# Kernel tuning notes

Hardware: AMD Instinct MI355X
Metric: run time of the kernel (lower is better)

## Reference

```python
import jax, jax.numpy as jnp
import numpy as np

EPS = 1e-5
K = 3          # deform conv kernel size
N = K * K      # 9 sampling points per output pixel


def conv2d(x, w, b=None):
    # x [B,C,H,W], w [O,I,kh,kw], stride 1, SAME padding (== torch padding=k//2)
    y = jax.lax.conv_general_dilated(x, w, (1, 1), 'SAME',
                                     dimension_numbers=('NCHW', 'OIHW', 'NCHW'))
    if b is not None:
        y = y + b[None, :, None, None]
    return y


def bilinear_sample(img, y, x):
    # img [B,C,H,W]; y,x [B,N,H,W] float sampling coordinates; zero padding outside.
    B, C, H, W = img.shape
    y0 = jnp.floor(y); x0 = jnp.floor(x)
    wy1 = y - y0; wy0 = 1.0 - wy1
    wx1 = x - x0; wx0 = 1.0 - wx1
    img_flat = img.reshape(B, C, H * W)

    def gather(yy, xx):
        valid = (yy >= 0) & (yy <= H - 1) & (xx >= 0) & (xx <= W - 1)
        yc = jnp.clip(yy, 0, H - 1).astype(jnp.int32)
        xc = jnp.clip(xx, 0, W - 1).astype(jnp.int32)
        idx = (yc * W + xc).reshape(B, -1)                      # [B, N*H*W]
        v = jax.vmap(lambda im, ix: im[:, ix])(img_flat, idx)   # [B, C, N*H*W]
        v = v.reshape(B, C, N, H, W)
        return v * valid[:, None].astype(img.dtype)

    v00 = gather(y0,     x0)
    v01 = gather(y0,     x0 + 1)
    v10 = gather(y0 + 1, x0)
    v11 = gather(y0 + 1, x0 + 1)
    wy0 = wy0[:, None]; wy1 = wy1[:, None]
    wx0 = wx0[:, None]; wx1 = wx1[:, None]
    return wy0 * (wx0 * v00 + wx1 * v01) + wy1 * (wx0 * v10 + wx1 * v11)


def deform_conv(x, w_off, b_off, w):
    # DeformConv2d(k=3, pad=1, stride=1, bias=False): offsets predicted by a 3x3 conv,
    # per-pixel bilinear sampling at p0 + pn + offset, then 3x3 weighted sum.
    B, C, H, W = x.shape
    off = conv2d(x, w_off, b_off)               # [B, 2N, H, W]
    dy, dx = off[:, :N], off[:, N:]
    ky, kx = jnp.meshgrid(jnp.arange(K) - 1, jnp.arange(K) - 1, indexing='ij')
    ky = ky.reshape(N).astype(x.dtype)
    kx = kx.reshape(N).astype(x.dtype)
    ii = jnp.arange(H, dtype=x.dtype)[None, None, :, None]
    jj = jnp.arange(W, dtype=x.dtype)[None, None, None, :]
    ysamp = ii + ky[None, :, None, None] + dy   # [B,N,H,W]
    xsamp = jj + kx[None, :, None, None] + dx
    s = bilinear_sample(x, ysamp, xsamp)        # [B,C,N,H,W]
    Cout = w.shape[0]
    return jnp.einsum('bcnhw,ocn->bohw', s, w.reshape(Cout, C, N))


def batchnorm_relu(x, gamma, beta):
    # train-mode BatchNorm2d (batch statistics, biased variance) + ReLU
    m = x.mean(axis=(0, 2, 3), keepdims=True)
    v = x.var(axis=(0, 2, 3), keepdims=True)
    xn = (x - m) * jax.lax.rsqrt(v + EPS)
    return jax.nn.relu(xn * gamma[None, :, None, None] + beta[None, :, None, None])


def maxpool2(x):
    return jax.lax.reduce_window(x, -jnp.inf, jax.lax.max,
                                 (1, 1, 2, 2), (1, 1, 2, 2), 'VALID')


def setup_inputs() -> dict:
    key = jax.random.key(0)
    ks = jax.random.split(key, 16)
    B, Cin, Cout, H, W = 4, 32, 64, 256, 256
    Hp, Wp = H // 2, W // 2
    f = jax.random.normal
    inp = {
        'x':  f(ks[0], (B, Cin, H, W), jnp.float32),
        'h0': f(ks[1], (B, Cout, Hp, Wp), jnp.float32),
        'c0': f(ks[2], (B, Cout, Hp, Wp), jnp.float32),
        # deform conv 1: Cin -> Cout
        'w_off1': f(ks[3], (2 * N, Cin, K, K), jnp.float32) * 0.01,
        'b_off1': jnp.zeros((2 * N,), jnp.float32),
        'w1': f(ks[4], (Cout, Cin, K, K), jnp.float32) * 0.05,
        'g1': jnp.ones((Cout,), jnp.float32),
        'be1': jnp.zeros((Cout,), jnp.float32),
        # deform conv 2: Cout -> Cout
        'w_off2': f(ks[5], (2 * N, Cout, K, K), jnp.float32) * 0.01,
        'b_off2': jnp.zeros((2 * N,), jnp.float32),
        'w2': f(ks[6], (Cout, Cout, K, K), jnp.float32) * 0.05,
        'g2': jnp.ones((Cout,), jnp.float32),
        'be2': jnp.zeros((Cout,), jnp.float32),
        # ConvLSTM gates: conv(cat(x, h)) -> 4*hidden channels
        'w_gates': f(ks[7], (4 * Cout, 2 * Cout, K, K), jnp.float32) * 0.05,
        'b_gates': jnp.zeros((4 * Cout,), jnp.float32),
    }
    return inp


def reference(x, h0, c0, w_off1, b_off1, w1, g1, be1,
              w_off2, b_off2, w2, g2, be2, w_gates, b_gates):
    # maxpool_conv = MaxPool2d(2) -> DoubleDConv (deform conv + BN + ReLU, twice)
    x = maxpool2(x)
    x = batchnorm_relu(deform_conv(x, w_off1, b_off1, w1), g1, be1)
    x = batchnorm_relu(deform_conv(x, w_off2, b_off2, w2), g2, be2)
    # ConvLSTM cell
    gates = conv2d(jnp.concatenate([x, h0], axis=1), w_gates, b_gates)
    i, f, o, g = jnp.split(gates, 4, axis=1)
    c = jax.nn.sigmoid(f) * c0 + jax.nn.sigmoid(i) * jnp.tanh(g)
    h = jax.nn.sigmoid(o) * jnp.tanh(c)
    # module returns (x, state) with x == hidden, state == (hidden, cell)
    return h, c
```

## Files before the change

### kernel.cpp

```cpp
#include <hip/hip_runtime.h>
#include <hip/hip_fp16.h>
#include <math.h>

#define P 128
#define NP (P*P)
#define BATCH 4

typedef __attribute__((ext_vector_type(8))) short bf16x8;
typedef __attribute__((ext_vector_type(8))) _Float16 h16x8;
typedef __attribute__((ext_vector_type(4))) float f32x4;

__device__ __forceinline__ float sigmoidf_(float x){ return 1.f/(1.f+__expf(-x)); }
__device__ __forceinline__ float tanhf_(float x){
  float ax = fabsf(x);
  float e = __expf(2.f*ax);
  float t = 1.f - 2.f/(e + 1.f);
  return copysignf(t, x);
}
__device__ __forceinline__ short f2bf(float f){
  unsigned u = __builtin_bit_cast(unsigned, f);
  u = (u + 0x7FFFu + ((u>>16)&1u)) >> 16;
  return (short)u;
}
__device__ __forceinline__ short f2h(float f){
  return (short)__half_as_short(__float2half(f));
}

__global__ void prep_k(const float* __restrict__ x, float* __restrict__ xp,
                       const float* __restrict__ wg, const float* __restrict__ w1,
                       const float* __restrict__ w2, const float* __restrict__ wo1,
                       const float* __restrict__ wo2,
                       short* __restrict__ wA, short* __restrict__ wd1T,
                       short* __restrict__ wd2T, short* __restrict__ woT1,
                       short* __restrict__ woT2){
  int bx = blockIdx.x;
  if (bx < 256){
    int idx = bx*256 + threadIdx.x;
    int wp = idx & (P-1); int t = idx >> 7; int hp = t & (P-1); int b = t >> 7;
    const float* src = x + ((size_t)b*32*65536) + (size_t)(hp*2)*256 + wp*2;
    float m[32];
    #pragma unroll
    for (int c = 0; c < 32; c++){
      const float* s = src + (size_t)c*65536;
      float2 t0 = *(const float2*)s;
      float2 t1 = *(const float2*)(s + 256);
      m[c] = fmaxf(fmaxf(t0.x, t0.y), fmaxf(t1.x, t1.y));
    }
    float* dst = xp + (size_t)idx*32;
    #pragma unroll
    for (int q = 0; q < 8; q++) *(float4*)(dst + q*4) = *(float4*)(m + q*4);
    return;
  }
  int idx = (bx - 256)*256 + threadIdx.x;
  if (idx < 294912){
    int s = idx & 7; int l = (idx>>3) & 63; int mb = (idx>>9) & 15;
    int cb = (idx>>13) & 3; int tap = idx >> 15;
    int ln = l & 15, kg = l >> 4;
    int r = mb*16 + ln; int ch = r >> 2, gate = r & 3;
    int cin = cb*32 + kg*8 + s;
    wA[idx] = f2bf(wg[((size_t)(gate*64 + ch)*128 + cin)*9 + tap]);
    return;
  }
  idx -= 294912;
  if (idx < 18432){
    int s = idx & 7; int l = (idx>>3) & 63; int mb = (idx>>9) & 3; int tap = idx >> 11;
    int ln = l & 15, kg = l >> 4;
    int o = mb*16 + ln; int cin = kg*8 + s;
    wd1T[idx] = f2h(w1[((size_t)(o*32 + cin))*9 + tap]);
    return;
  }
  idx -= 18432;
  if (idx < 36864){
    int s = idx & 7; int l = (idx>>3) & 63; int mb = (idx>>9) & 3;
    int cb = (idx>>11) & 1; int tap = idx >> 12;
    int ln = l & 15, kg = l >> 4;
    int o = mb*16 + ln; int cin = cb*32 + kg*8 + s;
    wd2T[idx] = f2h(w2[((size_t)(o*64 + cin))*9 + tap]);
    return;
  }
  idx -= 36864;
  if (idx < 9216){
    int s = idx & 7; int l = (idx>>3) & 63; int mb = (idx>>9) & 1; int tap = idx >> 10;
    int ln = l & 15, kg = l >> 4;
    int o = mb*16 + ln; int cin = kg*8 + s;
    woT1[idx] = (o < 18) ? f2h(wo1[((size_t)(o*32 + cin))*9 + tap]) : (short)0;
    return;
  }
  idx -= 9216;
  if (idx < 18432){
    int s = idx & 7; int l = (idx>>3) & 63; int mb = (idx>>9) & 1;
    int cb = (idx>>10) & 1; int tap = idx >> 11;
    int ln = l & 15, kg = l >> 4;
    int o = mb*16 + ln; int cin = cb*32 + kg*8 + s;
    woT2[idx] = (o < 18) ? f2h(wo2[((size_t)(o*64 + cin))*9 + tap]) : (short)0;
  }
}

template<int CIN, bool BNIN>
__global__ __launch_bounds__(256) void deform_fused_k(
    const float* __restrict__ incl, const float* __restrict__ bstats,
    const float* __restrict__ b_off,
    const short* __restrict__ woT, const short* __restrict__ wdT,
    float* __restrict__ outcl, float* __restrict__ part){
  const int HS = 14, NHP = HS*HS;
  const int ROWB = CIN*2;
  const int CG = CIN/8, CGS = (CIN==64)?3:2;
  const int PM = (CIN==64)?7:3;
  const int NCB = CIN/32;
  __shared__ short xt[NHP*CIN];
  __shared__ float off_lds[64][20];
  __shared__ float red_s[4][64], red_q[4][64];
  int tid = threadIdx.x;
  int tile = blockIdx.x, b = blockIdx.y;
  int tx0 = (tile & 15)*8, ty0 = (tile >> 4)*8;
  const float* inb = incl + (size_t)b*NP*CIN;
  for (int e = tid; e < NHP*CG; e += 256){
    int cg = e & (CG-1), p = e >> CGS;
    int hr = p/HS, wc = p - hr*HS;
    int gy = ty0 + hr - 3, gx = tx0 + wc - 3;
    union { short s[8]; __half2 h[4]; h16x8 v; } u;
    if (((unsigned)gy < P) && ((unsigned)gx < P)){
      const float* src = inb + ((size_t)gy*P + gx)*CIN + cg*8;
      float4 a = *(const float4*)src, bb = *(const float4*)(src+4);
      if (BNIN){
        int c = cg*8;
        a.x = fmaxf(a.x*bstats[c+0]+bstats[64+c+0], 0.f);
        a.y = fmaxf(a.y*bstats[c+1]+bstats[64+c+1], 0.f);
        a.z = fmaxf(a.z*bstats[c+2]+bstats[64+c+2], 0.f);
        a.w = fmaxf(a.w*bstats[c+3]+bstats[64+c+3], 0.f);
        bb.x = fmaxf(bb.x*bstats[c+4]+bstats[64+c+4], 0.f);
        bb.y = fmaxf(bb.y*bstats[c+5]+bstats[64+c+5], 0.f);
        bb.z = fmaxf(bb.z*bstats[c+6]+bstats[64+c+6], 0.f);
        bb.w = fmaxf(bb.w*bstats[c+7]+bstats[64+c+7], 0.f);
      }
      u.h[0] = __float22half2_rn(float2{a.x, a.y});
      u.h[1] = __float22half2_rn(float2{a.z, a.w});
      u.h[2] = __float22half2_rn(float2{bb.x, bb.y});
      u.h[3] = __float22half2_rn(float2{bb.z, bb.w});
    } else {
      #pragma unroll
      for (int j = 0; j < 8; j++) u.s[j] = 0;
    }
    *(h16x8*)((char*)xt + p*ROWB + ((cg*16) ^ ((p & PM)<<4))) = u.v;
  }
  __syncthreads();

  int lane = tid & 63, wid = tid >> 6;
  int kg = lane >> 4, ln = lane & 15;
  int py = ty0 + wid*2 + (ln>>3), pxg = tx0 + (ln&7);
  int pl = wid*16 + ln;

  {
    f32x4 acc_o[2];
    acc_o[0] = (f32x4){0.f,0.f,0.f,0.f};
    acc_o[1] = (f32x4){0.f,0.f,0.f,0.f};
    #pragma unroll
    for (int tap = 0; tap < 9; tap++){
      int ky = tap/3, kx = tap - (tap/3)*3;
      int lr = wid*2 + (ln>>3) + ky + 2;
      int lc = (ln&7) + kx + 2;
      int p = lr*HS + lc;
      #pragma unroll
      for (int cb = 0; cb < NCB; cb++){
        h16x8 bfv = *(const h16x8*)((const char*)xt + p*ROWB + (((cb*64) + kg*16) ^ ((p & PM)<<4)));
        h16x8 af0 = *(const h16x8*)(const void*)(woT + ((size_t)((tap*NCB + cb)*2 + 0)*512 + lane*8));
        h16x8 af1 = *(const h16x8*)(const void*)(woT + ((size_t)((tap*NCB + cb)*2 + 1)*512 + lane*8));
        acc_o[0] = __builtin_amdgcn_mfma_f32_16x16x32_f16(af0, bfv, acc_o[0], 0, 0, 0);
        acc_o[1] = __builtin_amdgcn_mfma_f32_16x16x32_f16(af1, bfv, acc_o[1], 0, 0, 0);
      }
    }
    #pragma unroll
    for (int mf = 0; mf < 2; mf++){
      #pragma unroll
      for (int j = 0; j < 4; j++){
        int o = mf*16 + kg*4 + j;
        if (o < 18) off_lds[pl][o] = acc_o[mf][j] + b_off[o];
      }
    }
  }
  __syncthreads();

  f32x4 acc[4];
  #pragma unroll
  for (int mf = 0; mf < 4; mf++) acc[mf] = (f32x4){0.f,0.f,0.f,0.f};

  for (int tap = 0; tap < 9; tap++){
    float dy = off_lds[pl][tap], dx = off_lds[pl][9+tap];
    float ys = (float)(py + tap/3 - 1) + dy;
    float xs = (float)(pxg + tap%3 - 1) + dx;
    float y0f = floorf(ys), x0f = floorf(xs);
    float wy1 = ys - y0f, wx1 = xs - x0f;
    float wy0 = 1.f - wy1, wx0 = 1.f - wx1;
    int y0 = (int)y0f, x0 = (int)x0f;
    bool v0y = ((unsigned)y0 < P), v1y = ((unsigned)(y0+1) < P);
    bool v0x = ((unsigned)x0 < P), v1x = ((unsigned)(x0+1) < P);
    float w00 = (v0y && v0x) ? wy0*wx0 : 0.f;
    float w01 = (v0y && v1x) ? wy0*wx1 : 0.f;
    float w10 = (v1y && v0x) ? wy1*wx0 : 0.f;
    float w11 = (v1y && v1x) ? wy1*wx1 : 0.f;
    __half2 w00h = __float2half2_rn(w00);
    __half2 w01h = __float2half2_rn(w01);
    __half2 w10h = __float2half2_rn(w10);
    __half2 w11h = __float2half2_rn(w11);
    int ly0 = min(max(y0 - ty0 + 3, 0), HS-1);
    int ly1 = min(max(y0 + 1 - ty0 + 3, 0), HS-1);
    int lx0 = min(max(x0 - tx0 + 3, 0), HS-1);
    int lx1 = min(max(x0 + 1 - tx0 + 3, 0), HS-1);
    int p00 = ly0*HS + lx0, p01 = ly0*HS + lx1;
    int p10 = ly1*HS + lx0, p11 = ly1*HS + lx1;
    #pragma unroll
    for (int cb = 0; cb < NCB; cb++){
      int ko = (cb*32 + kg*8)*2;
      union { __half2 h[4]; h16x8 v; } c00, c01, c10, c11, bu;
      c00.v = *(const h16x8*)((const char*)xt + p00*ROWB + (ko ^ ((p00 & PM)<<4)));
      c01.v = *(const h16x8*)((const char*)xt + p01*ROWB + (ko ^ ((p01 & PM)<<4)));
      c10.v = *(const h16x8*)((const char*)xt + p10*ROWB + (ko ^ ((p10 & PM)<<4)));
      c11.v = *(const h16x8*)((const char*)xt + p11*ROWB + (ko ^ ((p11 & PM)<<4)));
      #pragma unroll
      for (int j = 0; j < 4; j++){
        bu.h[j] = __hfma2(c00.h[j], w00h,
                  __hfma2(c01.h[j], w01h,
                  __hfma2(c10.h[j], w10h,
                  __hmul2(c11.h[j], w11h))));
      }
      #pragma unroll
      for (int mf = 0; mf < 4; mf++){
        h16x8 af = *(const h16x8*)(const void*)(wdT + ((size_t)((tap*NCB + cb)*4 + mf)*512 + lane*8));
        acc[mf] = __builtin_amdgcn_mfma_f32_16x16x32_f16(af, bu.v, acc[mf], 0, 0, 0);
      }
    }
  }
  #pragma unroll
  for (int mf = 0; mf < 4; mf++){
    float* dst = outcl + ((size_t)b*NP + (size_t)py*P + pxg)*64 + mf*16 + kg*4;
    *(f32x4*)dst = acc[mf];
  }

  #pragma unroll
  for (int mf = 0; mf < 4; mf++){
    #pragma unroll
    for (int j = 0; j < 4; j++){
      float s = acc[mf][j], q = s*s;
      #pragma unroll
      for (int o = 1; o < 16; o <<= 1){
        s += __shfl_xor(s, o);
        q += __shfl_xor(q, o);
      }
      if (ln == 0){
        int ch = mf*16 + kg*4 + j;
        red_s[wid][ch] = s;
        red_q[wid][ch] = q;
      }
    }
  }
  __syncthreads();
  int blk = b*256 + tile;
  if (tid < 128){
    int ch = tid & 63;
    float v = (tid < 64)
      ? (red_s[0][ch]+red_s[1][ch]+red_s[2][ch]+red_s[3][ch])
      : (red_q[0][ch]+red_q[1][ch]+red_q[2][ch]+red_q[3][ch]);
    part[(size_t)tid*1024 + blk] = v;
  }
}

__global__ void bnfinal2_k(const float* __restrict__ part, const float* __restrict__ g,
                           const float* __restrict__ be, float* __restrict__ stats){
  int ch = blockIdx.x;
  int tid = threadIdx.x;
  float S = 0.f, Q = 0.f;
  for (int i = tid; i < 1024; i += 256){
    S += part[(size_t)ch*1024 + i];
    Q += part[(size_t)(64+ch)*1024 + i];
  }
  __shared__ float rs[256], rq[256];
  rs[tid] = S; rq[tid] = Q;
  __syncthreads();
  for (int o = 128; o > 0; o >>= 1){
    if (tid < o){ rs[tid] += rs[tid+o]; rq[tid] += rq[tid+o]; }
    __syncthreads();
  }
  if (tid == 0){
    const float inv = 1.f/(float)(BATCH*NP);
    float mean = rs[0]*inv;
    float var = rq[0]*inv - mean*mean;
    float scale = rsqrtf(var + 1e-5f)*g[ch];
    stats[ch] = scale;
    stats[64+ch] = be[ch] - mean*scale;
  }
}

__global__ void aux1_k(const float* __restrict__ part, const float* __restrict__ g,
                       const float* __restrict__ be, float* __restrict__ stats,
                       const float* __restrict__ h0, short* __restrict__ hcl){
  int bx = blockIdx.x;
  int tid = threadIdx.x;
  if (bx < 64){
    int ch = bx;
    float S = 0.f, Q = 0.f;
    for (int i = tid; i < 1024; i += 256){
      S += part[(size_t)ch*1024 + i];
      Q += part[(size_t)(64+ch)*1024 + i];
    }
    __shared__ float rs[256], rq[256];
    rs[tid] = S; rq[tid] = Q;
    __syncthreads();
    for (int o = 128; o > 0; o >>= 1){
      if (tid < o){ rs[tid] += rs[tid+o]; rq[tid] += rq[tid+o]; }
      __syncthreads();
    }
    if (tid == 0){
      const float inv = 1.f/(float)(BATCH*NP);
      float mean = rs[0]*inv;
      float var = rq[0]*inv - mean*mean;
      float scale = rsqrtf(var + 1e-5f)*g[ch];
      stats[ch] = scale;
      stats[64+ch] = be[ch] - mean*scale;
    }
    return;
  }
  {
    __shared__ float t[64][65];
    int blk = bx - 64;
    int b = blk >> 8;
    int p0 = (blk & 255)*64;
    int pl = tid & 63;
    int cq = tid >> 6;
    const float* src = h0 + (size_t)b*64*NP + p0 + pl;
    #pragma unroll
    for (int i = 0; i < 16; i++)
      t[cq*16+i][pl] = src[(size_t)(cq*16+i)*NP];
    __syncthreads();
    int p = tid >> 2, q = tid & 3;
    short* dst = hcl + ((size_t)(b*NP + p0 + p))*64 + q*16;
    union { short s[8]; bf16x8 v; } o0, o1;
    #pragma unroll
    for (int i = 0; i < 8; i++){ o0.s[i] = f2bf(t[q*16+i][p]); o1.s[i] = f2bf(t[q*16+8+i][p]); }
    *(bf16x8*)dst = o0.v;
    *(bf16x8*)(dst+8) = o1.v;
  }
}

__global__ __launch_bounds__(512, 4) void gates_mfma_k(
    const float* __restrict__ y2, const float* __restrict__ stats,
    const short* __restrict__ hcl, const float* __restrict__ c0,
    const short* __restrict__ wA, const float* __restrict__ bg,
    float* __restrict__ outh, float* __restrict__ outc){
  extern __shared__ short lds[];
  short* bs = lds;
  short* abuf = lds + 180*128;
  int tid = threadIdx.x;
  int tile = blockIdx.x, b = blockIdx.y;
  int tx0 = (tile & 7)*16, ty0 = (tile >> 3)*8;
  int lane = tid & 63, wid = tid >> 6;

  for (int e = tid; e < 180*16; e += 512){
    int cg = e & 15, p = e >> 4;
    int hr = p/18, wc = p - hr*18;
    int gy = ty0 + hr - 1, gx = tx0 + wc - 1;
    union { short s[8]; bf16x8 v; } u;
    if (((unsigned)gy < P) && ((unsigned)gx < P)){
      if (cg < 8){
        const float* src = y2 + ((size_t)(b*NP) + (size_t)gy*P + gx)*64 + cg*8;
        float4 a = *(const float4*)src, b4 = *(const float4*)(src+4);
        int c = cg*8;
        u.s[0] = f2bf(fmaxf(a.x*stats[c+0]+stats[64+c+0], 0.f));
        u.s[1] = f2bf(fmaxf(a.y*stats[c+1]+stats[64+c+1], 0.f));
        u.s[2] = f2bf(fmaxf(a.z*stats[c+2]+stats[64+c+2], 0.f));
        u.s[3] = f2bf(fmaxf(a.w*stats[c+3]+stats[64+c+3], 0.f));
        u.s[4] = f2bf(fmaxf(b4.x*stats[c+4]+stats[64+c+4], 0.f));
        u.s[5] = f2bf(fmaxf(b4.y*stats[c+5]+stats[64+c+5], 0.f));
        u.s[6] = f2bf(fmaxf(b4.z*stats[c+6]+stats[64+c+6], 0.f));
        u.s[7] = f2bf(fmaxf(b4.w*stats[c+7]+stats[64+c+7], 0.f));
      } else {
        u.v = *(const bf16x8*)(hcl + ((size_t)(b*NP) + (size_t)gy*P + gx)*64 + (cg-8)*8);
      }
    } else {
      #pragma unroll
      for (int j = 0; j < 8; j++) u.s[j] = 0;
    }
    *(bf16x8*)((char*)bs + p*256 + ((cg*16) ^ ((p&7)<<4))) = u.v;
  }

  auto stageA = [&](int c, int bi){
    const short* g = wA + (size_t)c*8192;
    short* l = abuf + bi*8192;
    #pragma unroll
    for (int i = 0; i < 2; i++){
      int unit = wid*2 + i;
      __builtin_amdgcn_global_load_lds(
          (const __attribute__((address_space(1))) unsigned int*)(g + (size_t)(unit*64 + lane)*8),
          (__attribute__((address_space(3))) unsigned int*)(l + (size_t)unit*512),
          16, 0, 0);
    }
  };

  stageA(0, 0);
  stageA(1, 1);
  __syncthreads();

  int kg = lane >> 4, ln = lane & 15;
  int ct = wid >> 1, nh = wid & 1;
  f32x4 acc[4][4];
  #pragma unroll
  for (int mf = 0; mf < 4; mf++)
    #pragma unroll
    for (int rr = 0; rr < 4; rr++) acc[mf][rr] = (f32x4){0.f,0.f,0.f,0.f};

  for (int c = 0; c < 36; c++){
    int cur = c & 1;
    int tap = c >> 2, cb = c & 3;
    int ky = tap/3, kx = tap - ky*3;
    const short* al = abuf + cur*8192;
    bf16x8 af[4], bf[4];
    #pragma unroll
    for (int mf = 0; mf < 4; mf++)
      af[mf] = *(const bf16x8*)(al + (size_t)(ct*4 + mf)*512 + lane*8);
    #pragma unroll
    for (int rr = 0; rr < 4; rr++){
      int p = (nh*4 + rr + ky)*18 + ln + kx;
      bf[rr] = *(const bf16x8*)((const char*)bs + p*256 + (((cb*64) + kg*16) ^ ((p&7)<<4)));
    }
    asm volatile("s_waitcnt lgkmcnt(0)" ::: "memory");
    __builtin_amdgcn_sched_barrier(0);
    __builtin_amdgcn_s_setprio(1);
    #pragma unroll
    for (int rr = 0; rr < 4; rr++)
      #pragma unroll
      for (int mf = 0; mf < 4; mf++)
        acc[mf][rr] = __builtin_amdgcn_mfma_f32_16x16x32_bf16(af[mf], bf[rr], acc[mf][rr], 0, 0, 0);
    __builtin_amdgcn_s_setprio(0);
    asm volatile("s_waitcnt vmcnt(0)" ::: "memory");
    __builtin_amdgcn_sched_barrier(0);
    __builtin_amdgcn_s_barrier();
    __builtin_amdgcn_sched_barrier(0);
    if (c + 2 < 36) stageA(c + 2, cur);
  }

  #pragma unroll
  for (int mf = 0; mf < 4; mf++){
    int ch = ct*16 + mf*4 + kg;
    float bi = bg[ch], bff = bg[64+ch], bo = bg[128+ch], bgv = bg[192+ch];
    #pragma unroll
    for (int rr = 0; rr < 4; rr++){
      int py = ty0 + nh*4 + rr, px = tx0 + ln;
      size_t pidx = ((size_t)(b*64 + ch))*NP + (size_t)py*P + px;
      f32x4 a = acc[mf][rr];
      float cv = sigmoidf_(a[1]+bff)*c0[pidx] + sigmoidf_(a[0]+bi)*tanhf_(a[3]+bgv);
      float hv = sigmoidf_(a[2]+bo)*tanhf_(cv);
      outh[pidx] = hv;
      outc[pidx] = cv;
    }
  }
}

extern "C" void kernel_launch(void* const* d_in, const int* in_sizes, int n_in,
                              void* d_out, int out_size, void* d_ws, size_t ws_size,
                              hipStream_t stream) {
  const float* x      = (const float*)d_in[0];
  const float* h0     = (const float*)d_in[1];
  const float* c0     = (const float*)d_in[2];
  const float* w_off1 = (const float*)d_in[3];
  const float* b_off1 = (const float*)d_in[4];
  const float* w1     = (const float*)d_in[5];
  const float* g1     = (const float*)d_in[6];
  const float* be1    = (const float*)d_in[7];
  const float* w_off2 = (const float*)d_in[8];
  const float* b_off2 = (const float*)d_in[9];
  const float* w2     = (const float*)d_in[10];
  const float* g2     = (const float*)d_in[11];
  const float* be2    = (const float*)d_in[12];
  const float* wg     = (const float*)d_in[13];
  const float* bg     = (const float*)d_in[14];

  float* ws     = (float*)d_ws;
  float* xpcl   = ws;
  short* hcl    = (short*)ws;
  float* y1     = ws + 2097152;
  float* y2     = ws + 6291456;
  float* part   = ws + 10485760;
  float* stats1 = ws + 10616832;
  float* stats2 = ws + 10616960;
  short* wA     = (short*)(ws + 10617088);
  short* wd1T   = wA + 294912;
  short* wd2T   = wd1T + 18432;
  short* woT1   = wd2T + 36864;
  short* woT2   = woT1 + 9216;

  (void)hipFuncSetAttribute((const void*)gates_mfma_k,
                            hipFuncAttributeMaxDynamicSharedMemorySize, 78848);

  prep_k<<<dim3(256 + 1476), dim3(256), 0, stream>>>(
      x, xpcl, wg, w1, w2, w_off1, w_off2, wA, wd1T, wd2T, woT1, woT2);

  deform_fused_k<32,false><<<dim3(256, BATCH), dim3(256), 0, stream>>>(
      xpcl, stats1, b_off1, woT1, wd1T, y1, part);
  aux1_k<<<dim3(64 + 1024), dim3(256), 0, stream>>>(part, g1, be1, stats1, h0, hcl);

  deform_fused_k<64,true><<<dim3(256, BATCH), dim3(256), 0, stream>>>(
      y1, stats1, b_off2, woT2, wd2T, y2, part);
  bnfinal2_k<<<dim3(64), dim3(256), 0, stream>>>(part, g2, be2, stats2);

  float* outh = (float*)d_out;
  float* outc = outh + (size_t)BATCH*64*NP;
  gates_mfma_k<<<dim3(128, BATCH), dim3(512), 78848, stream>>>(
      y2, stats2, hcl, c0, wA, bg, outh, outc);
}
```

Measured before the change: 118.0 us.

## Store deform-conv intermediates in bf16 and double-step gates MFMA pipeline

The two deform-conv outputs are now written as bf16 instead of fp32. The second deform kernel and the gates kernel read them as bf16, which halves the intermediate global traffic and workspace. The gates GEMM loop now processes two K-chunks per iteration, staging both A buffers after one barrier, to cut barrier count. This adds bf16 rounding of pre-BN activations, which may slightly change accuracy.

```diff
diff --git a/kernel.cpp b/kernel.cpp
--- a/kernel.cpp
+++ b/kernel.cpp
@@ -7,6 +7,7 @@
 #define BATCH 4
 
 typedef __attribute__((ext_vector_type(8))) short bf16x8;
+typedef __attribute__((ext_vector_type(4))) short s16x4;
 typedef __attribute__((ext_vector_type(8))) _Float16 h16x8;
 typedef __attribute__((ext_vector_type(4))) float f32x4;
 
@@ -21,6 +22,10 @@
   unsigned u = __builtin_bit_cast(unsigned, f);
   u = (u + 0x7FFFu + ((u>>16)&1u)) >> 16;
   return (short)u;
+}
+__device__ __forceinline__ float bf2f(short s){
+  unsigned u = ((unsigned)(unsigned short)s) << 16;
+  return __builtin_bit_cast(float, u);
 }
 __device__ __forceinline__ short f2h(float f){
   return (short)__half_as_short(__float2half(f));
@@ -96,12 +101,12 @@
   }
 }
 
-template<int CIN, bool BNIN>
+template<int CIN, bool BNIN, bool INBF16>
 __global__ __launch_bounds__(256) void deform_fused_k(
-    const float* __restrict__ incl, const float* __restrict__ bstats,
+    const void* __restrict__ incl, const float* __restrict__ bstats,
     const float* __restrict__ b_off,
     const short* __restrict__ woT, const short* __restrict__ wdT,
-    float* __restrict__ outcl, float* __restrict__ part){
+    short* __restrict__ outb, float* __restrict__ part){
   const int HS = 14, NHP = HS*HS;
   const int ROWB = CIN*2;
   const int CG = CIN/8, CGS = (CIN==64)?3:2;
@@ -113,30 +118,33 @@
   int tid = threadIdx.x;
   int tile = blockIdx.x, b = blockIdx.y;
   int tx0 = (tile & 15)*8, ty0 = (tile >> 4)*8;
-  const float* inb = incl + (size_t)b*NP*CIN;
   for (int e = tid; e < NHP*CG; e += 256){
     int cg = e & (CG-1), p = e >> CGS;
     int hr = p/HS, wc = p - hr*HS;
     int gy = ty0 + hr - 3, gx = tx0 + wc - 3;
     union { short s[8]; __half2 h[4]; h16x8 v; } u;
     if (((unsigned)gy < P) && ((unsigned)gx < P)){
-      const float* src = inb + ((size_t)gy*P + gx)*CIN + cg*8;
-      float4 a = *(const float4*)src, bb = *(const float4*)(src+4);
+      float v[8];
+      if (INBF16){
+        const short* src = (const short*)incl + ((size_t)b*NP + (size_t)gy*P + gx)*CIN + cg*8;
+        bf16x8 raw = *(const bf16x8*)src;
+        #pragma unroll
+        for (int j = 0; j < 8; j++) v[j] = bf2f(raw[j]);
+      } else {
+        const float* src = (const float*)incl + ((size_t)b*NP + (size_t)gy*P + gx)*CIN + cg*8;
+        float4 a = *(const float4*)src, bb = *(const float4*)(src+4);
+        v[0]=a.x; v[1]=a.y; v[2]=a.z; v[3]=a.w;
+        v[4]=bb.x; v[5]=bb.y; v[6]=bb.z; v[7]=bb.w;
+      }
       if (BNIN){
         int c = cg*8;
-        a.x = fmaxf(a.x*bstats[c+0]+bstats[64+c+0], 0.f);
-        a.y = fmaxf(a.y*bstats[c+1]+bstats[64+c+1], 0.f);
-        a.z = fmaxf(a.z*bstats[c+2]+bstats[64+c+2], 0.f);
-        a.w = fmaxf(a.w*bstats[c+3]+bstats[64+c+3], 0.f);
-        bb.x = fmaxf(bb.x*bstats[c+4]+bstats[64+c+4], 0.f);
-        bb.y = fmaxf(bb.y*bstats[c+5]+bstats[64+c+5], 0.f);
-        bb.z = fmaxf(bb.z*bstats[c+6]+bstats[64+c+6], 0.f);
-        bb.w = fmaxf(bb.w*bstats[c+7]+bstats[64+c+7], 0.f);
-      }
-      u.h[0] = __float22half2_rn(float2{a.x, a.y});
-      u.h[1] = __float22half2_rn(float2{a.z, a.w});
-      u.h[2] = __float22half2_rn(float2{bb.x, bb.y});
-      u.h[3] = __float22half2_rn(float2{bb.z, bb.w});
+        #pragma unroll
+        for (int j = 0; j < 8; j++) v[j] = fmaxf(v[j]*bstats[c+j]+bstats[64+c+j], 0.f);
+      }
+      u.h[0] = __float22half2_rn(float2{v[0], v[1]});
+      u.h[1] = __float22half2_rn(float2{v[2], v[3]});
+      u.h[2] = __float22half2_rn(float2{v[4], v[5]});
+      u.h[3] = __float22half2_rn(float2{v[6], v[7]});
     } else {
       #pragma unroll
       for (int j = 0; j < 8; j++) u.s[j] = 0;
@@ -232,8 +240,11 @@
   }
   #pragma unroll
   for (int mf = 0; mf < 4; mf++){
-    float* dst = outcl + ((size_t)b*NP + (size_t)py*P + pxg)*64 + mf*16 + kg*4;
-    *(f32x4*)dst = acc[mf];
+    short* dst = outb + ((size_t)b*NP + (size_t)py*P + pxg)*64 + mf*16 + kg*4;
+    s16x4 o;
+    #pragma unroll
+    for (int j = 0; j < 4; j++) o[j] = f2bf(acc[mf][j]);
+    *(s16x4*)dst = o;
   }
 
   #pragma unroll
@@ -342,7 +353,7 @@
 }
 
 __global__ __launch_bounds__(512, 4) void gates_mfma_k(
-    const float* __restrict__ y2, const float* __restrict__ stats,
+    const short* __restrict__ y2b, const float* __restrict__ stats,
     const short* __restrict__ hcl, const float* __restrict__ c0,
     const short* __restrict__ wA, const float* __restrict__ bg,
     float* __restrict__ outh, float* __restrict__ outc){
@@ -361,17 +372,14 @@
     union { short s[8]; bf16x8 v; } u;
     if (((unsigned)gy < P) && ((unsigned)gx < P)){
       if (cg < 8){
-        const float* src = y2 + ((size_t)(b*NP) + (size_t)gy*P + gx)*64 + cg*8;
-        float4 a = *(const float4*)src, b4 = *(const float4*)(src+4);
+        const short* src = y2b + ((size_t)(b*NP) + (size_t)gy*P + gx)*64 + cg*8;
+        bf16x8 raw = *(const bf16x8*)src;
         int c = cg*8;
-        u.s[0] = f2bf(fmaxf(a.x*stats[c+0]+stats[64+c+0], 0.f));
-        u.s[1] = f2bf(fmaxf(a.y*stats[c+1]+stats[64+c+1], 0.f));
-        u.s[2] = f2bf(fmaxf(a.z*stats[c+2]+stats[64+c+2], 0.f));
-        u.s[3] = f2bf(fmaxf(a.w*stats[c+3]+stats[64+c+3], 0.f));
-        u.s[4] = f2bf(fmaxf(b4.x*stats[c+4]+stats[64+c+4], 0.f));
-        u.s[5] = f2bf(fmaxf(b4.y*stats[c+5]+stats[64+c+5], 0.f));
-        u.s[6] = f2bf(fmaxf(b4.z*stats[c+6]+stats[64+c+6], 0.f));
-        u.s[7] = f2bf(fmaxf(b4.w*stats[c+7]+stats[64+c+7], 0.f));
+        #pragma unroll
+        for (int j = 0; j < 8; j++){
+          float v = fmaxf(bf2f(raw[j])*stats[c+j] + stats[64+c+j], 0.f);
+          u.s[j] = f2bf(v);
+        }
       } else {
         u.v = *(const bf16x8*)(hcl + ((size_t)(b*NP) + (size_t)gy*P + gx)*64 + (cg-8)*8);
       }
@@ -407,19 +415,38 @@
     #pragma unroll
     for (int rr = 0; rr < 4; rr++) acc[mf][rr] = (f32x4){0.f,0.f,0.f,0.f};
 
-  for (int c = 0; c < 36; c++){
-    int cur = c & 1;
-    int tap = c >> 2, cb = c & 3;
-    int ky = tap/3, kx = tap - ky*3;
-    const short* al = abuf + cur*8192;
-    bf16x8 af[4], bf[4];
-    #pragma unroll
-    for (int mf = 0; mf < 4; mf++)
-      af[mf] = *(const bf16x8*)(al + (size_t)(ct*4 + mf)*512 + lane*8);
+  for (int cc = 0; cc < 36; cc += 2){
+    int tap0 = cc >> 2, cb0 = cc & 3;
+    int tap1 = (cc+1) >> 2, cb1 = (cc+1) & 3;
+    int ky0 = tap0/3, kx0 = tap0 - ky0*3;
+    int ky1 = tap1/3, kx1 = tap1 - ky1*3;
+    bf16x8 af0[4], af1[4], bf0[4], bf1[4];
+    #pragma unroll
+    for (int mf = 0; mf < 4; mf++){
+      af0[mf] = *(const bf16x8*)(abuf + (size_t)(ct*4 + mf)*512 + lane*8);
+      af1[mf] = *(const bf16x8*)(abuf + 8192 + (size_t)(ct*4 + mf)*512 + lane*8);
+    }
     #pragma unroll
     for (int rr = 0; rr < 4; rr++){
-      int p = (nh*4 + rr + ky)*18 + ln + kx;
-      bf[rr] = *(const bf16x8*)((const char*)bs + p*256 + (((cb*64) + kg*16) ^ ((p&7)<<4)));
+      int p = (nh*4 + rr + ky0)*18 + ln + kx0;
+      bf0[rr] = *(const bf16x8*)((const char*)bs + p*256 + (((cb0*64) + kg*16) ^ ((p&7)<<4)));
+    }
+    asm volatile("s_waitcnt lgkmcnt(0)" ::: "memory");
+    __builtin_amdgcn_sched_barrier(0);
+    __builtin_amdgcn_s_barrier();
+    __builtin_amdgcn_sched_barrier(0);
+    if (cc + 2 < 36){ stageA(cc + 2, 0); stageA(cc + 3, 1); }
+    __builtin_amdgcn_s_setprio(1);
+    #pragma unroll
+    for (int rr = 0; rr < 4; rr++)
+      #pragma unroll
+      for (int mf = 0; mf < 4; mf++)
+        acc[mf][rr] = __builtin_amdgcn_mfma_f32_16x16x32_bf16(af0[mf], bf0[rr], acc[mf][rr], 0, 0, 0);
+    __builtin_amdgcn_s_setprio(0);
+    #pragma unroll
+    for (int rr = 0; rr < 4; rr++){
+      int p = (nh*4 + rr + ky1)*18 + ln + kx1;
+      bf1[rr] = *(const bf16x8*)((const char*)bs + p*256 + (((cb1*64) + kg*16) ^ ((p&7)<<4)));
     }
     asm volatile("s_waitcnt lgkmcnt(0)" ::: "memory");
     __builtin_amdgcn_sched_barrier(0);
@@ -428,13 +455,12 @@
     for (int rr = 0; rr < 4; rr++)
       #pragma unroll
       for (int mf = 0; mf < 4; mf++)
-        acc[mf][rr] = __builtin_amdgcn_mfma_f32_16x16x32_bf16(af[mf], bf[rr], acc[mf][rr], 0, 0, 0);
+        acc[mf][rr] = __builtin_amdgcn_mfma_f32_16x16x32_bf16(af1[mf], bf1[rr], acc[mf][rr], 0, 0, 0);
     __builtin_amdgcn_s_setprio(0);
     asm volatile("s_waitcnt vmcnt(0)" ::: "memory");
     __builtin_amdgcn_sched_barrier(0);
     __builtin_amdgcn_s_barrier();
     __builtin_amdgcn_sched_barrier(0);
-    if (c + 2 < 36) stageA(c + 2, cur);
   }
 
   #pragma unroll
@@ -476,12 +502,12 @@
   float* ws     = (float*)d_ws;
   float* xpcl   = ws;
   short* hcl    = (short*)ws;
-  float* y1     = ws + 2097152;
-  float* y2     = ws + 6291456;
-  float* part   = ws + 10485760;
-  float* stats1 = ws + 10616832;
-  float* stats2 = ws + 10616960;
-  short* wA     = (short*)(ws + 10617088);
+  short* y1b    = (short*)(ws + 2097152);
+  short* y2b    = (short*)(ws + 4194304);
+  float* part   = ws + 6291456;
+  float* stats1 = ws + 6422528;
+  float* stats2 = ws + 6422656;
+  short* wA     = (short*)(ws + 6422784);
   short* wd1T   = wA + 294912;
   short* wd2T   = wd1T + 18432;
   short* woT1   = wd2T + 36864;
@@ -493,16 +519,16 @@
   prep_k<<<dim3(256 + 1476), dim3(256), 0, stream>>>(
       x, xpcl, wg, w1, w2, w_off1, w_off2, wA, wd1T, wd2T, woT1, woT2);
 
-  deform_fused_k<32,false><<<dim3(256, BATCH), dim3(256), 0, stream>>>(
-      xpcl, stats1, b_off1, woT1, wd1T, y1, part);
+  deform_fused_k<32,false,false><<<dim3(256, BATCH), dim3(256), 0, stream>>>(
+      xpcl, stats1, b_off1, woT1, wd1T, y1b, part);
   aux1_k<<<dim3(64 + 1024), dim3(256), 0, stream>>>(part, g1, be1, stats1, h0, hcl);
 
-  deform_fused_k<64,true><<<dim3(256, BATCH), dim3(256), 0, stream>>>(
-      y1, stats1, b_off2, woT2, wd2T, y2, part);
+  deform_fused_k<64,true,true><<<dim3(256, BATCH), dim3(256), 0, stream>>>(
+      y1b, stats1, b_off2, woT2, wd2T, y2b, part);
   bnfinal2_k<<<dim3(64), dim3(256), 0, stream>>>(part, g2, be2, stats2);
 
   float* outh = (float*)d_out;
   float* outc = outh + (size_t)BATCH*64*NP;
   gates_mfma_k<<<dim3(128, BATCH), dim3(512), 78848, stream>>>(
-      y2, stats2, hcl, c0, wA, bg, outh, outc);
-}
+      y2b, stats2, hcl, c0, wA, bg, outh, outc);
+}
```

After: 142.6 us. +20.9%, slower.
